# Performance work log

Hardware: AMD Instinct MI355X
Metric: run time of the kernel (lower is better)

## Reference

```python
import jax, jax.numpy as jnp
import numpy as np

B, T, D, HID, H = 256, 256, 72, 512, 1024


def setup_inputs() -> dict:
    key = jax.random.key(0)
    ks = jax.random.split(key, 21)
    s = 0.02
    w = lambda k, sh: jax.random.normal(k, sh, dtype=jnp.float32) * s
    return {
        "x": jax.random.normal(ks[0], (B, T, D), dtype=jnp.float32),
        "to_predict": 10,
        "p2l_w1": w(ks[1], (HID, D)), "p2l_b1": jnp.zeros((HID,), jnp.float32),
        "p2l_w2": w(ks[2], (H, HID)), "p2l_b2": jnp.zeros((H,), jnp.float32),
        "enc_wih": w(ks[3], (3 * H, H)), "enc_whh": w(ks[4], (3 * H, H)),
        "enc_bih": jnp.zeros((3 * H,), jnp.float32), "enc_bhh": jnp.zeros((3 * H,), jnp.float32),
        "dec_wih": w(ks[5], (3 * H, H)), "dec_whh": w(ks[6], (3 * H, H)),
        "dec_bih": jnp.zeros((3 * H,), jnp.float32), "dec_bhh": jnp.zeros((3 * H,), jnp.float32),
        "l2p_w1": w(ks[7], (HID, H)), "l2p_b1": jnp.zeros((HID,), jnp.float32),
        "l2p_w2": w(ks[8], (D, HID)), "l2p_b2": jnp.zeros((D,), jnp.float32),
        "l2s_w1": w(ks[9], (HID, H)), "l2s_b1": jnp.zeros((HID,), jnp.float32),
        "l2s_w2": w(ks[10], (1, HID)), "l2s_b2": jnp.zeros((1,), jnp.float32),
    }


def _lin(x, w, b):
    return x @ w.T + b


def _gru_gates(gi, gh, h):
    # PyTorch gate order: reset, update, new
    i_r, i_z, i_n = jnp.split(gi, 3, axis=-1)
    h_r, h_z, h_n = jnp.split(gh, 3, axis=-1)
    r = jax.nn.sigmoid(i_r + h_r)
    z = jax.nn.sigmoid(i_z + h_z)
    n = jnp.tanh(i_n + r * h_n)
    return (1.0 - z) * n + z * h


def _forward(x, to_predict,
             p2l_w1, p2l_b1, p2l_w2, p2l_b2,
             enc_wih, enc_whh, enc_bih, enc_bhh,
             dec_wih, dec_whh, dec_bih, dec_bhh,
             l2p_w1, l2p_b1, l2p_w2, l2p_b2,
             l2s_w1, l2s_b1, l2s_w2, l2s_b2):
    par2lat = lambda p: jax.nn.relu(_lin(jax.nn.relu(_lin(p, p2l_w1, p2l_b1)), p2l_w2, p2l_b2))
    lat2par = lambda h: _lin(jax.nn.relu(_lin(h, l2p_w1, l2p_b1)), l2p_w2, l2p_b2)

    latent = par2lat(x)  # [B,T,H]
    # encoder GRU (batch_first, single layer, h0 = 0)
    xp = _lin(latent, enc_wih, enc_bih)  # [B,T,3H] precomputed input projections

    def enc_step(h, gi_t):
        h2 = _gru_gates(gi_t, _lin(h, enc_whh, enc_bhh), h)
        return h2, h2

    h0 = jnp.zeros((x.shape[0], H), latent.dtype)
    _, out = jax.lax.scan(enc_step, h0, jnp.swapaxes(xp, 0, 1))
    output = jnp.swapaxes(out, 0, 1)  # [B,T,H]

    # softmax attention pooling over time
    logits = _lin(jax.nn.relu(_lin(output, l2s_w1, l2s_b1)), l2s_w2, l2s_b2)  # [B,T,1]
    weights = jax.nn.softmax(logits, axis=1)
    Rep = jnp.sum(weights * output, axis=1)  # [B,H]

    def dec_step(carry, _):
        hs, p = carry
        inp = par2lat(p)
        hs = _gru_gates(_lin(inp, dec_wih, dec_bih), _lin(hs, dec_whh, dec_bhh), hs)
        pred = lat2par(hs)
        return (hs, pred), pred

    _, preds = jax.lax.scan(dec_step, (Rep, x[:, -1, :]), None, length=to_predict)
    return jnp.transpose(preds, (1, 0, 2)), Rep  # [B,to_predict,72], [B,H]


def reference(x, to_predict,
              p2l_w1, p2l_b1, p2l_w2, p2l_b2,
              enc_wih, enc_whh, enc_bih, enc_bhh,
              dec_wih, dec_whh, dec_bih, dec_bhh,
              l2p_w1, l2p_b1, l2p_w2, l2p_b2,
              l2s_w1, l2s_b1, l2s_w2, l2s_b2):
    return _forward(x, to_predict,
                    p2l_w1, p2l_b1, p2l_w2, p2l_b2,
                    enc_wih, enc_whh, enc_bih, enc_bhh,
                    dec_wih, dec_whh, dec_bih, dec_bhh,
                    l2p_w1, l2p_b1, l2p_w2, l2p_b2,
                    l2s_w1, l2s_b1, l2s_w2, l2s_b2)
```

## Files before the change

### kernel.cpp

```cpp
#include <hip/hip_runtime.h>
#include <hip/hip_bf16.h>
#include <cstdint>
#include <cstddef>


using bf16 = __hip_bfloat16;
typedef __attribute__((ext_vector_type(8))) short short8;
typedef __attribute__((ext_vector_type(4))) short s4_t;
typedef __attribute__((ext_vector_type(4))) float floatx4;

#define B_    256
#define T_    256
#define D_    72
#define DP_   96
#define HID_  512
#define H_    1024
#define H3_   3072
#define NPRED 10
#define CHUNK 32
#define RA    16384

__device__ __forceinline__ float b2f(bf16 v){ return __bfloat162float(v); }
__device__ __forceinline__ bf16  f2b(float v){ return __float2bfloat16(v); }

__device__ __forceinline__ void async_ld16(const bf16* g, bf16* l) {
  __builtin_amdgcn_global_load_lds(
      (const __attribute__((address_space(1))) unsigned int*)g,
      (__attribute__((address_space(3))) unsigned int*)l,
      16, 0, 0);
}

__device__ __forceinline__ short8 load16_cached(const bf16* p) {
  short8 r;
  asm volatile("global_load_dwordx4 %0, %1, off"
               : "=v"(r) : "v"(p) : "memory");
  return r;
}
__device__ __forceinline__ void store8_llc(bf16* p, s4_t v) {
  asm volatile("global_store_dwordx2 %0, %1, off sc0 sc1"
               :: "v"(p), "v"(v) : "memory");
}

enum { EPI_F32 = 0, EPI_BF16 = 1, EPI_BF16_RELU = 2, EPI_BF16_RELU_PERM = 3 };

template<int BM, int BN, int WM, int WN, int EPI>
__global__ __launch_bounds__(256, 2) void gemm_bt(
    const bf16* __restrict__ A, const bf16* __restrict__ B,
    const float* __restrict__ bias, void* __restrict__ Cout,
    int M, int N, int K, int row_off)
{
  constexpr int BK = 32;
  constexpr int NWN = BN / WN;
  constexpr int MT = WM / 16, NT = WN / 16;
  constexpr int ASEG = BM * 4;
  constexpr int TSEG = (BM + BN) * 4;
  static_assert((BM/WM)*(BN/WN) == 4, "4 waves");
  static_assert(TSEG % 256 == 0, "uniform staging");

  __shared__ __align__(16) bf16 smem[(BM + BN) * BK];
  bf16* As = smem;
  bf16* Bs = smem + BM * BK;

  const int tid  = threadIdx.x;
  const int lane = tid & 63;
  const int wave = tid >> 6;
  const int wm = wave / NWN, wn = wave % NWN;
  const int m0 = blockIdx.y * BM, n0 = blockIdx.x * BN;

  floatx4 acc[MT][NT];
#pragma unroll
  for (int i = 0; i < MT; i++)
#pragma unroll
    for (int j = 0; j < NT; j++)
      acc[i][j] = floatx4{0.f, 0.f, 0.f, 0.f};

  const int krow = (lane >> 4) << 3;
  const int r16  = lane & 15;

  for (int k0 = 0; k0 < K; k0 += BK) {
    __syncthreads();
#pragma unroll
    for (int it = 0; it < TSEG / 256; it++) {
      int s = tid + it * 256;
      const bf16* g;
      if (s < ASEG) {
        int row = s >> 2, kseg = s & 3;
        g = A + (size_t)(m0 + row) * K + k0 + kseg * 8;
      } else {
        int s2 = s - ASEG;
        int row = s2 >> 2, kseg = s2 & 3;
        g = B + (size_t)(n0 + row) * K + k0 + kseg * 8;
      }
      async_ld16(g, smem + (size_t)s * 8);
    }
    __syncthreads();
    short8 af[MT], bfr[NT];
#pragma unroll
    for (int i = 0; i < MT; i++)
      af[i] = *(const short8*)(As + (wm * WM + i * 16 + r16) * BK + krow);
#pragma unroll
    for (int j = 0; j < NT; j++)
      bfr[j] = *(const short8*)(Bs + (wn * WN + j * 16 + r16) * BK + krow);
#pragma unroll
    for (int i = 0; i < MT; i++)
#pragma unroll
      for (int j = 0; j < NT; j++)
        acc[i][j] = __builtin_amdgcn_mfma_f32_16x16x32_bf16(af[i], bfr[j], acc[i][j], 0, 0, 0);
  }

#pragma unroll
  for (int i = 0; i < MT; i++) {
#pragma unroll
    for (int j = 0; j < NT; j++) {
      int gn = n0 + wn * WN + j * 16 + r16;
      float bv = bias ? bias[gn] : 0.f;
#pragma unroll
      for (int r = 0; r < 4; r++) {
        int gm = m0 + wm * WM + i * 16 + ((lane >> 4) << 2) + r;
        float v = acc[i][j][r] + bv;
        if (EPI == EPI_BF16_RELU || EPI == EPI_BF16_RELU_PERM) v = fmaxf(v, 0.f);
        size_t orow;
        if (EPI == EPI_BF16_RELU_PERM) {
          int g = row_off + gm;
          orow = (size_t)(g & 255) * 256 + (size_t)(g >> 8);
        } else {
          orow = (size_t)gm;
        }
        if (EPI == EPI_F32) ((float*)Cout)[orow * (size_t)N + gn] = v;
        else                ((bf16*) Cout)[orow * (size_t)N + gn] = f2b(v);
      }
    }
  }
}

__global__ __launch_bounds__(256, 2) void gemm_bt_dual(
    const bf16* __restrict__ A0, const bf16* __restrict__ B0,
    const float* __restrict__ bias0, float* __restrict__ C0,
    const bf16* __restrict__ A1, const bf16* __restrict__ B1,
    const float* __restrict__ bias1, float* __restrict__ C1,
    int M, int N, int K)
{
  constexpr int BM = 64, BN = 128, BK = 32;
  constexpr int ASEG = BM * 4, TSEG = (BM + BN) * 4;
  const bf16* A = blockIdx.z ? A1 : A0;
  const bf16* B = blockIdx.z ? B1 : B0;
  const float* bias = blockIdx.z ? bias1 : bias0;
  float* Cout = blockIdx.z ? C1 : C0;

  __shared__ __align__(16) bf16 smem[(BM + BN) * BK];
  bf16* As = smem;
  bf16* Bs = smem + BM * BK;

  const int tid  = threadIdx.x;
  const int lane = tid & 63;
  const int wave = tid >> 6;
  const int wm = wave >> 1, wn = wave & 1;
  const int m0 = blockIdx.y * BM, n0 = blockIdx.x * BN;

  floatx4 acc[2][4];
#pragma unroll
  for (int i = 0; i < 2; i++)
#pragma unroll
    for (int j = 0; j < 4; j++)
      acc[i][j] = floatx4{0.f, 0.f, 0.f, 0.f};

  const int krow = (lane >> 4) << 3;
  const int r16  = lane & 15;

  for (int k0 = 0; k0 < K; k0 += BK) {
    __syncthreads();
#pragma unroll
    for (int it = 0; it < TSEG / 256; it++) {
      int s = tid + it * 256;
      const bf16* g;
      if (s < ASEG) {
        int row = s >> 2, kseg = s & 3;
        g = A + (size_t)(m0 + row) * K + k0 + kseg * 8;
      } else {
        int s2 = s - ASEG;
        int row = s2 >> 2, kseg = s2 & 3;
        g = B + (size_t)(n0 + row) * K + k0 + kseg * 8;
      }
      async_ld16(g, smem + (size_t)s * 8);
    }
    __syncthreads();
    short8 af[2], bfr[4];
#pragma unroll
    for (int i = 0; i < 2; i++)
      af[i] = *(const short8*)(As + (wm * 32 + i * 16 + r16) * BK + krow);
#pragma unroll
    for (int j = 0; j < 4; j++)
      bfr[j] = *(const short8*)(Bs + (wn * 64 + j * 16 + r16) * BK + krow);
#pragma unroll
    for (int i = 0; i < 2; i++)
#pragma unroll
      for (int j = 0; j < 4; j++)
        acc[i][j] = __builtin_amdgcn_mfma_f32_16x16x32_bf16(af[i], bfr[j], acc[i][j], 0, 0, 0);
  }

#pragma unroll
  for (int i = 0; i < 2; i++)
#pragma unroll
    for (int j = 0; j < 4; j++) {
      int gn = n0 + wn * 64 + j * 16 + r16;
      float bv = bias[gn];
#pragma unroll
      for (int r = 0; r < 4; r++) {
        int gm = m0 + wm * 32 + i * 16 + ((lane >> 4) << 2) + r;
        Cout[(size_t)gm * N + gn] = acc[i][j][r] + bv;
      }
    }
}

__global__ __launch_bounds__(256, 2) void score_gemm(
    const bf16* __restrict__ A,
    const bf16* __restrict__ Bw,
    const float* __restrict__ b1,
    const float* __restrict__ w2,
    float* __restrict__ part)
{
  constexpr int BK = 32;
  __shared__ __align__(16) bf16 smem[(128 + 128) * BK];
  __shared__ float pl[128][33];
  bf16* As = smem;
  bf16* Bs = smem + 128 * BK;

  const int tid  = threadIdx.x;
  const int lane = tid & 63;
  const int wave = tid >> 6;
  const int wm = wave >> 1, wn = wave & 1;
  const int m0 = blockIdx.y * 128, n0 = blockIdx.x * 128;
  const int krow = (lane >> 4) << 3;
  const int r16  = lane & 15;
  const int kq   = lane >> 4;

  floatx4 acc[4][4];
#pragma unroll
  for (int i = 0; i < 4; i++)
#pragma unroll
    for (int j = 0; j < 4; j++)
      acc[i][j] = floatx4{0.f, 0.f, 0.f, 0.f};

  for (int k0 = 0; k0 < H_; k0 += BK) {
    __syncthreads();
#pragma unroll
    for (int it = 0; it < 4; it++) {
      int s = tid + it * 256;
      const bf16* g;
      if (s < 512) {
        int row = s >> 2, kseg = s & 3;
        g = A + (size_t)(m0 + row) * H_ + k0 + kseg * 8;
      } else {
        int s2 = s - 512;
        int row = s2 >> 2, kseg = s2 & 3;
        g = Bw + (size_t)(n0 + row) * H_ + k0 + kseg * 8;
      }
      async_ld16(g, smem + (size_t)s * 8);
    }
    __syncthreads();
    short8 af[4], bfr[4];
#pragma unroll
    for (int i = 0; i < 4; i++)
      af[i] = *(const short8*)(As + (wm * 64 + i * 16 + r16) * BK + krow);
#pragma unroll
    for (int j = 0; j < 4; j++)
      bfr[j] = *(const short8*)(Bs + (wn * 64 + j * 16 + r16) * BK + krow);
#pragma unroll
    for (int i = 0; i < 4; i++)
#pragma unroll
      for (int j = 0; j < 4; j++)
        acc[i][j] = __builtin_amdgcn_mfma_f32_16x16x32_bf16(af[i], bfr[j], acc[i][j], 0, 0, 0);
  }

#pragma unroll
  for (int i = 0; i < 4; i++) {
#pragma unroll
    for (int r = 0; r < 4; r++) {
      int row = wm * 64 + i * 16 + kq * 4 + r;
      float s = 0.f;
#pragma unroll
      for (int j = 0; j < 4; j++) {
        int gn = n0 + wn * 64 + j * 16 + r16;
        s += fmaxf(acc[i][j][r] + b1[gn], 0.f) * w2[gn];
      }
      pl[row][wn * 16 + r16] = s;
    }
  }
  __syncthreads();
  if (tid < 128) {
    float t = 0.f;
#pragma unroll
    for (int c = 0; c < 32; c++) t += pl[tid][c];
    part[(size_t)(m0 + tid) * 4 + blockIdx.x] = t;
  }
}

__global__ void logits_red(const float* __restrict__ part, float* __restrict__ logit)
{
  int i = blockIdx.x * blockDim.x + threadIdx.x;
  logit[i] = part[(size_t)i * 4] + part[(size_t)i * 4 + 1]
           + part[(size_t)i * 4 + 2] + part[(size_t)i * 4 + 3];
}

__global__ void convert_pad(const float* __restrict__ in, bf16* __restrict__ out,
                            int rows, int kin, int kout)
{
  size_t idx = (size_t)blockIdx.x * blockDim.x + threadIdx.x;
  if (idx >= (size_t)rows * kout) return;
  int r = idx / kout, c = idx % kout;
  out[idx] = (c < kin) ? f2b(in[(size_t)r * kin + c]) : f2b(0.f);
}

__global__ void enc_init(float* __restrict__ h32, unsigned* __restrict__ bar)
{
  int idx = blockIdx.x * blockDim.x + threadIdx.x;
  h32[idx] = 0.f;
  if (idx < 512) bar[idx] = 0u;
}

__global__ void ppad_init(const float* __restrict__ x, bf16* __restrict__ ppad)
{
  int idx = blockIdx.x * blockDim.x + threadIdx.x;
  int b = idx / DP_, c = idx % DP_;
  float v = (c < D_) ? x[((size_t)b * T_ + (T_ - 1)) * D_ + c] : 0.f;
  ppad[idx] = f2b(v);
}

__device__ __forceinline__ float sigm(float v){ return 1.f / (1.f + __expf(-v)); }

#define ENC_SMEM (98304 + 4*64*52*4)
static_assert(ENC_SMEM <= 160*1024, "LDS");

__global__ __launch_bounds__(256, 1) void enc_fused(
    const bf16* __restrict__ xpc_cur,
    const bf16* __restrict__ whh,
    const float* __restrict__ bhh,
    bf16* __restrict__ enc_out,
    float* __restrict__ h32g,
    unsigned* __restrict__ bar,
    int t0,
    const bf16* __restrict__ lat_nxt,
    const bf16* __restrict__ wih,
    const float* __restrict__ bih,
    bf16* __restrict__ xpc_nxt)
{
  extern __shared__ char smem[];
  const int tid  = threadIdx.x;
  const int lane = tid & 63;
  const int wave = tid >> 6;
  const int wg   = blockIdx.x;
  const int r16  = lane & 15;
  const int kq   = lane >> 4;

  if (wg < 128) {
    float* P = (float*)(smem + 98304);
    constexpr int PS = 52;

    const int rgrp = wg >> 5;
    const int rowb = rgrp * 64;
    const int j0   = (wg & 31) * 32;
    const int kb0  = wave * 256;

    unsigned* flagp  = bar + rgrp * 32 + wave * 8 + (lane & 7);
    unsigned* myflag = bar + rgrp * 32 + (wg & 31);

    for (int ci = tid; ci < 48 * 128; ci += 256) {
      int wrow = ci >> 7, kslot = ci & 127;
      int g = wrow >> 4, jj = wrow & 15;
      short8 v = *(const short8*)(whh + ((size_t)(g * H_ + j0 + jj)) * H_ + kslot * 8);
      *(short8*)(smem + kslot * 768 + wrow * 16) = v;
    }
    short8 rw[8][3];
#pragma unroll
    for (int it = 0; it < 8; it++)
#pragma unroll
      for (int g = 0; g < 3; g++)
        rw[it][g] = *(const short8*)(whh + ((size_t)(g * H_ + j0 + 16 + r16)) * H_
                                     + kb0 + it * 32 + kq * 8);

    const int row_loc = tid >> 2;
    const int cq      = tid & 3;
    const int b       = rowb + row_loc;
    const int jb0     = j0 + cq * 4;
    const int jb1     = j0 + 16 + cq * 4;

    floatx4 h32r0 = *(const floatx4*)(h32g + (size_t)b * H_ + jb0);
    floatx4 h32r1 = *(const floatx4*)(h32g + (size_t)b * H_ + jb1);
    const floatx4 bhr0 = *(const floatx4*)(bhh + jb0);
    const floatx4 bhz0 = *(const floatx4*)(bhh + H_ + jb0);
    const floatx4 bhn0 = *(const floatx4*)(bhh + 2 * H_ + jb0);
    const floatx4 bhr1 = *(const floatx4*)(bhh + jb1);
    const floatx4 bhz1 = *(const floatx4*)(bhh + H_ + jb1);
    const floatx4 bhn1 = *(const floatx4*)(bhh + 2 * H_ + jb1);

    __syncthreads();

#define ISSUE(IT)                                                              \
    {                                                                          \
      _Pragma("unroll")                                                        \
      for (int rf = 0; rf < 4; rf++)                                           \
        a[(IT) & 3][rf] = load16_cached(hsrc + (size_t)(rowb + rf * 16 + r16) * H_ \
                                        + kb0 + (IT) * 32 + kq * 8);           \
    }
#define GRP(IT, WC)                                                            \
    do {                                                                       \
      const char* bb = smem + (wave * 32 + (IT) * 4 + kq) * 768 + r16 * 16;    \
      short8 bw0 = *(const short8*)(bb);                                       \
      short8 bw1 = *(const short8*)(bb + 256);                                 \
      short8 bw2 = *(const short8*)(bb + 512);                                 \
      asm volatile("s_waitcnt vmcnt(" #WC ")" ::: "memory");                   \
      __builtin_amdgcn_sched_barrier(0);                                       \
      _Pragma("unroll")                                                        \
      for (int rf = 0; rf < 4; rf++) {                                         \
        accA[rf][0] = __builtin_amdgcn_mfma_f32_16x16x32_bf16(a[(IT)&3][rf], bw0, accA[rf][0], 0, 0, 0); \
        accA[rf][1] = __builtin_amdgcn_mfma_f32_16x16x32_bf16(a[(IT)&3][rf], bw1, accA[rf][1], 0, 0, 0); \
        accA[rf][2] = __builtin_amdgcn_mfma_f32_16x16x32_bf16(a[(IT)&3][rf], bw2, accA[rf][2], 0, 0, 0); \
        accB[rf][0] = __builtin_amdgcn_mfma_f32_16x16x32_bf16(a[(IT)&3][rf], rw[IT][0], accB[rf][0], 0, 0, 0); \
        accB[rf][1] = __builtin_amdgcn_mfma_f32_16x16x32_bf16(a[(IT)&3][rf], rw[IT][1], accB[rf][1], 0, 0, 0); \
        accB[rf][2] = __builtin_amdgcn_mfma_f32_16x16x32_bf16(a[(IT)&3][rf], rw[IT][2], accB[rf][2], 0, 0, 0); \
      }                                                                        \
      if ((IT) + 4 < 8) ISSUE((IT) + 4)                                        \
    } while (0)

    for (int ts = 0; ts < CHUNK; ts++) {
      const int tg = t0 + ts;

      const bf16* gi = xpc_cur + ((size_t)ts * B_ + b) * H3_;
      s4_t vr0 = *(const s4_t*)(gi + jb0);
      s4_t vz0 = *(const s4_t*)(gi + H_ + jb0);
      s4_t vn0 = *(const s4_t*)(gi + 2 * H_ + jb0);
      s4_t vr1 = *(const s4_t*)(gi + jb1);
      s4_t vz1 = *(const s4_t*)(gi + H_ + jb1);
      s4_t vn1 = *(const s4_t*)(gi + 2 * H_ + jb1);

      floatx4 accA[4][3], accB[4][3];
#pragma unroll
      for (int rf = 0; rf < 4; rf++)
#pragma unroll
        for (int g = 0; g < 3; g++) {
          accA[rf][g] = floatx4{0.f, 0.f, 0.f, 0.f};
          accB[rf][g] = floatx4{0.f, 0.f, 0.f, 0.f};
        }

      if (tg > 0) {
        const unsigned tgt = (unsigned)tg;
        while (1) {
          unsigned f;
          asm volatile("global_load_dword %0, %1, off sc0 sc1"
                       : "=v"(f) : "v"(flagp) : "memory");
          asm volatile("s_waitcnt vmcnt(0)" ::: "memory");
          if (__all((int)(f >= tgt))) break;
          __builtin_amdgcn_s_sleep(2);
        }
        const bf16* hsrc = enc_out + (size_t)(tg - 1) * B_ * H_;
        short8 a[4][4];
        ISSUE(0) ISSUE(1) ISSUE(2) ISSUE(3)
        GRP(0, 12); GRP(1, 12); GRP(2, 12); GRP(3, 12);
        GRP(4, 12); GRP(5,  8); GRP(6,  4); GRP(7,  0);
      }

#pragma unroll
      for (int rf = 0; rf < 4; rf++)
#pragma unroll
        for (int g = 0; g < 3; g++)
#pragma unroll
          for (int rr = 0; rr < 4; rr++)
            P[(wave * 64 + rf * 16 + kq * 4 + rr) * PS + g * 16 + r16] = accA[rf][g][rr];
      __syncthreads();
      {
        const float* Pr = P + row_loc * PS + cq * 4;
        floatx4 sr4 = floatx4{0.f,0.f,0.f,0.f};
        floatx4 sz4 = floatx4{0.f,0.f,0.f,0.f};
        floatx4 sn4 = floatx4{0.f,0.f,0.f,0.f};
#pragma unroll
        for (int w = 0; w < 4; w++) {
          const float* pp = Pr + w * 64 * PS;
          sr4 += *(const floatx4*)(pp);
          sz4 += *(const floatx4*)(pp + 16);
          sn4 += *(const floatx4*)(pp + 32);
        }
        s4_t outv;
#pragma unroll
        for (int cc = 0; cc < 4; cc++) {
          float xr = __uint_as_float(((unsigned)(unsigned short)vr0[cc]) << 16);
          float xz = __uint_as_float(((unsigned)(unsigned short)vz0[cc]) << 16);
          float xn = __uint_as_float(((unsigned)(unsigned short)vn0[cc]) << 16);
          float rg = sigm(xr + sr4[cc] + bhr0[cc]);
          float zg = sigm(xz + sz4[cc] + bhz0[cc]);
          float ng = tanhf(xn + rg * (sn4[cc] + bhn0[cc]));
          float hnew = (1.f - zg) * ng + zg * h32r0[cc];
          h32r0[cc] = hnew;
          outv[cc] = (short)__builtin_bit_cast(unsigned short, f2b(hnew));
        }
        store8_llc(enc_out + ((size_t)tg * B_ + b) * H_ + jb0, outv);
      }
      __syncthreads();

#pragma unroll
      for (int rf = 0; rf < 4; rf++)
#pragma unroll
        for (int g = 0; g < 3; g++)
#pragma unroll
          for (int rr = 0; rr < 4; rr++)
            P[(wave * 64 + rf * 16 + kq * 4 + rr) * PS + g * 16 + r16] = accB[rf][g][rr];
      __syncthreads();
      {
        const float* Pr = P + row_loc * PS + cq * 4;
        floatx4 sr4 = floatx4{0.f,0.f,0.f,0.f};
        floatx4 sz4 = floatx4{0.f,0.f,0.f,0.f};
        floatx4 sn4 = floatx4{0.f,0.f,0.f,0.f};
#pragma unroll
        for (int w = 0; w < 4; w++) {
          const float* pp = Pr + w * 64 * PS;
          sr4 += *(const floatx4*)(pp);
          sz4 += *(const floatx4*)(pp + 16);
          sn4 += *(const floatx4*)(pp + 32);
        }
        s4_t outv;
#pragma unroll
        for (int cc = 0; cc < 4; cc++) {
          float xr = __uint_as_float(((unsigned)(unsigned short)vr1[cc]) << 16);
          float xz = __uint_as_float(((unsigned)(unsigned short)vz1[cc]) << 16);
          float xn = __uint_as_float(((unsigned)(unsigned short)vn1[cc]) << 16);
          float rg = sigm(xr + sr4[cc] + bhr1[cc]);
          float zg = sigm(xz + sz4[cc] + bhz1[cc]);
          float ng = tanhf(xn + rg * (sn4[cc] + bhn1[cc]));
          float hnew = (1.f - zg) * ng + zg * h32r1[cc];
          h32r1[cc] = hnew;
          outv[cc] = (short)__builtin_bit_cast(unsigned short, f2b(hnew));
        }
        store8_llc(enc_out + ((size_t)tg * B_ + b) * H_ + jb1, outv);
      }

      asm volatile("s_waitcnt vmcnt(0)" ::: "memory");
      __syncthreads();
      if (tid == 0) {
        unsigned v = (unsigned)(tg + 1);
        asm volatile("global_store_dword %0, %1, off sc0 sc1"
                     :: "v"(myflag), "v"(v) : "memory");
      }
    }
#undef GRP
#undef ISSUE

    *(floatx4*)(h32g + (size_t)b * H_ + jb0) = h32r0;
    *(floatx4*)(h32g + (size_t)b * H_ + jb1) = h32r1;

  } else {
    if (xpc_nxt == nullptr) return;
    const int p  = wg - 128;
    const int wm = wave >> 1, wn = wave & 1;
    bf16* As = (bf16*)smem;
    bf16* Bs = As + 128 * 32;
    const int krow = kq << 3;

    for (int tile = 0; tile < 12; tile++) {
      const int t  = p + tile * 128;
      const int m0 = (t / 24) * 128;
      const int n0 = (t % 24) * 128;

      floatx4 acc[4][4];
#pragma unroll
      for (int i = 0; i < 4; i++)
#pragma unroll
        for (int j = 0; j < 4; j++)
          acc[i][j] = floatx4{0.f, 0.f, 0.f, 0.f};

      for (int k0 = 0; k0 < H_; k0 += 32) {
        __syncthreads();
#pragma unroll
        for (int it = 0; it < 4; it++) {
          int s = tid + it * 256;
          const bf16* g;
          if (s < 512) {
            int row = s >> 2, kseg = s & 3;
            g = lat_nxt + (size_t)(m0 + row) * H_ + k0 + kseg * 8;
          } else {
            int s2 = s - 512;
            int row = s2 >> 2, kseg = s2 & 3;
            g = wih + (size_t)(n0 + row) * H_ + k0 + kseg * 8;
          }
          async_ld16(g, (bf16*)smem + (size_t)s * 8);
        }
        __syncthreads();
        short8 af[4], bfr[4];
#pragma unroll
        for (int i = 0; i < 4; i++)
          af[i] = *(const short8*)(As + (wm * 64 + i * 16 + r16) * 32 + krow);
#pragma unroll
        for (int j = 0; j < 4; j++)
          bfr[j] = *(const short8*)(Bs + (wn * 64 + j * 16 + r16) * 32 + krow);
#pragma unroll
        for (int i = 0; i < 4; i++)
#pragma unroll
          for (int j = 0; j < 4; j++)
            acc[i][j] = __builtin_amdgcn_mfma_f32_16x16x32_bf16(af[i], bfr[j], acc[i][j], 0, 0, 0);
      }

#pragma unroll
      for (int i = 0; i < 4; i++)
#pragma unroll
        for (int j = 0; j < 4; j++) {
          int gn = n0 + wn * 64 + j * 16 + r16;
          float bv = bih[gn];
#pragma unroll
          for (int r = 0; r < 4; r++) {
            int gm = m0 + wm * 64 + i * 16 + (kq << 2) + r;
            xpc_nxt[(size_t)gm * H3_ + gn] = f2b(acc[i][j][r] + bv);
          }
        }
      __syncthreads();
    }
  }
}

__global__ void dec_gates(const float* __restrict__ gi, const float* __restrict__ gh,
                          float* __restrict__ hs32, bf16* __restrict__ hs16)
{
  int idx = blockIdx.x * blockDim.x + threadIdx.x;
  int b = idx >> 10, j = idx & (H_ - 1);
  const float* gir = gi + (size_t)b * H3_;
  const float* ghr = gh + (size_t)b * H3_;
  float r = sigm(gir[j] + ghr[j]);
  float z = sigm(gir[j + H_] + ghr[j + H_]);
  float n = tanhf(gir[j + 2 * H_] + r * ghr[j + 2 * H_]);
  float hnew = (1.f - z) * n + z * hs32[idx];
  hs32[idx] = hnew;
  hs16[idx] = f2b(hnew);
}

__global__ void attention(const float* __restrict__ logits, const bf16* __restrict__ enc_out,
                          float* __restrict__ rep, float* __restrict__ hs32,
                          bf16* __restrict__ hs16)
{
  int b = blockIdx.x, t = threadIdx.x;
  __shared__ float w[T_];
  __shared__ float red[T_];
  float lg = logits[(size_t)t * B_ + b];
  red[t] = lg; __syncthreads();
  for (int s = 128; s > 0; s >>= 1) { if (t < s) red[t] = fmaxf(red[t], red[t + s]); __syncthreads(); }
  float mx = red[0]; __syncthreads();
  float e = __expf(lg - mx);
  w[t] = e; red[t] = e; __syncthreads();
  for (int s = 128; s > 0; s >>= 1) { if (t < s) red[t] += red[t + s]; __syncthreads(); }
  float inv = 1.f / red[0];
  float acc[4] = {0.f, 0.f, 0.f, 0.f};
  for (int tt = 0; tt < T_; tt++) {
    float wt = w[tt] * inv;
    const bf16* row = enc_out + ((size_t)tt * B_ + b) * H_;
#pragma unroll
    for (int i = 0; i < 4; i++) acc[i] += wt * b2f(row[t + i * 256]);
  }
#pragma unroll
  for (int i = 0; i < 4; i++) {
    int j = t + i * 256;
    rep [(size_t)b * H_ + j] = acc[i];
    hs32[(size_t)b * H_ + j] = acc[i];
    hs16[(size_t)b * H_ + j] = f2b(acc[i]);
  }
}

__global__ void pred_k(const bf16* __restrict__ e1, const float* __restrict__ w2,
                       const float* __restrict__ b2, float* __restrict__ out,
                       bf16* __restrict__ ppad, int s)
{
  int b = blockIdx.x, t = threadIdx.x;
  __shared__ float ev[HID_];
  for (int k = t; k < HID_; k += 256) ev[k] = b2f(e1[(size_t)b * HID_ + k]);
  __syncthreads();
  if (t < D_) {
    float acc = b2[t];
    const float* wr = w2 + (size_t)t * HID_;
    for (int k = 0; k < HID_; k++) acc += ev[k] * wr[k];
    out[(size_t)b * (NPRED * D_) + s * D_ + t] = acc;
    ppad[b * DP_ + t] = f2b(acc);
  }
}

extern "C" void kernel_launch(void* const* d_in, const int* in_sizes, int n_in,
                              void* d_out, int out_size, void* d_ws, size_t ws_size,
                              hipStream_t stream)
{
  const float* x       = (const float*)d_in[0];
  const float* p2l_w1  = (const float*)d_in[2];
  const float* p2l_b1  = (const float*)d_in[3];
  const float* p2l_w2  = (const float*)d_in[4];
  const float* p2l_b2  = (const float*)d_in[5];
  const float* enc_wih = (const float*)d_in[6];
  const float* enc_whh = (const float*)d_in[7];
  const float* enc_bih = (const float*)d_in[8];
  const float* enc_bhh = (const float*)d_in[9];
  const float* dec_wih = (const float*)d_in[10];
  const float* dec_whh = (const float*)d_in[11];
  const float* dec_bih = (const float*)d_in[12];
  const float* dec_bhh = (const float*)d_in[13];
  const float* l2p_w1  = (const float*)d_in[14];
  const float* l2p_b1  = (const float*)d_in[15];
  const float* l2p_w2  = (const float*)d_in[16];
  const float* l2p_b2  = (const float*)d_in[17];
  const float* l2s_w1  = (const float*)d_in[18];
  const float* l2s_b1  = (const float*)d_in[19];
  const float* l2s_w2  = (const float*)d_in[20];
  const float* l2s_b2  = (const float*)d_in[21];
  (void)l2s_b2;

  float* out_preds = (float*)d_out;
  float* out_rep   = (float*)d_out + (size_t)B_ * NPRED * D_;

  char* p = (char*)d_ws;
  auto alloc = [&](size_t bytes) -> char* {
    char* r = p; p += (bytes + 255) & ~(size_t)255; return r;
  };
  bf16* w_p2l1 = (bf16*)alloc((size_t)HID_ * DP_ * 2);
  bf16* w_p2l2 = (bf16*)alloc((size_t)H_ * HID_ * 2);
  bf16* w_ewih = (bf16*)alloc((size_t)H3_ * H_ * 2);
  bf16* w_ewhh = (bf16*)alloc((size_t)H3_ * H_ * 2);
  bf16* w_l2p1 = (bf16*)alloc((size_t)HID_ * H_ * 2);
  bf16* w_l2s1 = (bf16*)alloc((size_t)HID_ * H_ * 2);
  bf16* latent = (bf16*)alloc((size_t)B_ * T_ * H_ * 2);
  bf16* xpcA   = (bf16*)alloc((size_t)CHUNK * B_ * H3_ * 2);
  bf16* xpcB   = (bf16*)alloc((size_t)CHUNK * B_ * H3_ * 2);
  float* h32  = (float*)alloc((size_t)B_ * H_ * 4);
  float* hs32 = (float*)alloc((size_t)B_ * H_ * 4);
  bf16*  hs16 = (bf16*) alloc((size_t)B_ * H_ * 2);
  float* logit= (float*)alloc((size_t)B_ * T_ * 4);
  bf16*  d1   = (bf16*) alloc((size_t)B_ * HID_ * 2);
  bf16*  inp  = (bf16*) alloc((size_t)B_ * H_ * 2);
  bf16*  e1   = (bf16*) alloc((size_t)B_ * HID_ * 2);
  bf16*  ppad = (bf16*) alloc((size_t)B_ * DP_ * 2);
  unsigned* bar = (unsigned*)alloc(2048);
  bf16*  enc_out = latent;

  bf16* xb    = xpcB;
  bf16* tmpc  = xpcB + (size_t)B_ * T_ * DP_;
  float* part_g = (float*)xpcB;
  float* ghb  = (float*)(xpcA + (size_t)8 * 1024 * 1024);
  float* gib  = ghb + (size_t)B_ * H3_;
  bf16* w_dwih = xpcB;
  bf16* w_dwhh = xpcB + (size_t)H3_ * H_;

  if ((size_t)(p - (char*)d_ws) > ws_size) return;

  const int TB = B_ * T_;

  auto cgrid = [](size_t n) { return dim3((unsigned)((n + 255) / 256)); };
  convert_pad<<<cgrid((size_t)TB * DP_),   256, 0, stream>>>(x,       xb,     TB,   D_,   DP_);
  convert_pad<<<cgrid((size_t)HID_ * DP_), 256, 0, stream>>>(p2l_w1,  w_p2l1, HID_, D_,   DP_);
  convert_pad<<<cgrid((size_t)H_ * HID_),  256, 0, stream>>>(p2l_w2,  w_p2l2, H_,   HID_, HID_);
  convert_pad<<<cgrid((size_t)H3_ * H_),   256, 0, stream>>>(enc_wih, w_ewih, H3_,  H_,   H_);
  convert_pad<<<cgrid((size_t)H3_ * H_),   256, 0, stream>>>(enc_whh, w_ewhh, H3_,  H_,   H_);
  convert_pad<<<cgrid((size_t)HID_ * H_),  256, 0, stream>>>(l2p_w1,  w_l2p1, HID_, H_,   H_);
  convert_pad<<<cgrid((size_t)HID_ * H_),  256, 0, stream>>>(l2s_w1,  w_l2s1, HID_, H_,   H_);

  for (int rc = 0; rc < TB / RA; rc++) {
    { dim3 g(HID_ / 128, RA / 128);
      gemm_bt<128,128,64,64,EPI_BF16_RELU><<<g, 256, 0, stream>>>(
          xb + (size_t)rc * RA * DP_, w_p2l1, p2l_b1, tmpc, RA, HID_, DP_, 0); }
    { dim3 g(H_ / 128, RA / 128);
      gemm_bt<128,128,64,64,EPI_BF16_RELU_PERM><<<g, 256, 0, stream>>>(
          tmpc, w_p2l2, p2l_b2, latent, RA, H_, HID_, rc * RA); }
  }

  (void)hipFuncSetAttribute((const void*)enc_fused,
                            hipFuncAttributeMaxDynamicSharedMemorySize, ENC_SMEM);
  enc_init<<<(B_ * H_) / 256, 256, 0, stream>>>(h32, bar);
  { dim3 g(H3_ / 128, (CHUNK * B_) / 128);
    gemm_bt<128,128,64,64,EPI_BF16><<<g, 256, 0, stream>>>(
        latent, w_ewih, enc_bih, xpcA, CHUNK * B_, H3_, H_, 0); }
  for (int tc = 0; tc < T_ / CHUNK; tc++) {
    bf16* cur = (tc & 1) ? xpcB : xpcA;
    bf16* nxt = (tc < 7) ? ((tc & 1) ? xpcA : xpcB) : nullptr;
    const bf16* latn = latent + (size_t)(tc + 1 < 8 ? tc + 1 : 0) * CHUNK * B_ * H_;
    enc_fused<<<dim3(256), dim3(256), ENC_SMEM, stream>>>(
        cur, w_ewhh, enc_bhh, enc_out, h32, bar, tc * CHUNK,
        latn, w_ewih, enc_bih, nxt);
  }

  score_gemm<<<dim3(4, TB / 128), 256, 0, stream>>>(
      enc_out, w_l2s1, l2s_b1, l2s_w2, part_g);
  logits_red<<<TB / 256, 256, 0, stream>>>(part_g, logit);
  attention<<<B_, 256, 0, stream>>>(logit, enc_out, out_rep, hs32, hs16);

  convert_pad<<<cgrid((size_t)H3_ * H_), 256, 0, stream>>>(dec_wih, w_dwih, H3_, H_, H_);
  convert_pad<<<cgrid((size_t)H3_ * H_), 256, 0, stream>>>(dec_whh, w_dwhh, H3_, H_, H_);
  ppad_init<<<(B_ * DP_) / 256, 256, 0, stream>>>(x, ppad);
  for (int s = 0; s < NPRED; s++) {
    { dim3 g(HID_ / 128, B_ / 64);
      gemm_bt<64,128,32,64,EPI_BF16_RELU><<<g, 256, 0, stream>>>(ppad, w_p2l1, p2l_b1, d1, B_, HID_, DP_, 0); }
    { dim3 g(H_ / 128, B_ / 64);
      gemm_bt<64,128,32,64,EPI_BF16_RELU><<<g, 256, 0, stream>>>(d1, w_p2l2, p2l_b2, inp, B_, H_, HID_, 0); }
    { dim3 g(H3_ / 128, B_ / 64, 2);
      gemm_bt_dual<<<g, 256, 0, stream>>>(inp, w_dwih, dec_bih, gib,
                                          hs16, w_dwhh, dec_bhh, ghb, B_, H3_, H_); }
    dec_gates<<<(B_ * H_) / 256, 256, 0, stream>>>(gib, ghb, hs32, hs16);
    { dim3 g(HID_ / 128, B_ / 64);
      gemm_bt<64,128,32,64,EPI_BF16_RELU><<<g, 256, 0, stream>>>(hs16, w_l2p1, l2p_b1, e1, B_, HID_, H_, 0); }
    pred_k<<<B_, 256, 0, stream>>>(e1, l2p_w2, l2p_b2, out_preds, ppad, s);
  }
}
```

Measured before the change: 3.242 ms.

## Overlap attention score GEMM and decoder weight conversion with encoder recurrence

Producer blocks of the fused encoder kernel now compute the attention-score GEMM tiles for the previous chunk while consumer blocks run the recurrence. During the last chunk they also convert the decoder weights to bf16. This leaves only the final chunk's score tiles for a standalone launch, and the separate logits reduction is folded into the attention kernel. The aim is to hide score and conversion work behind the latency-bound GRU loop. The cost is that producer blocks get more work, which may delay the next chunk's input projections or contend for memory bandwidth with the recurrence.

```diff
diff --git a/kernel.cpp b/kernel.cpp
--- a/kernel.cpp
+++ b/kernel.cpp
@@ -212,24 +212,19 @@
     }
 }
 
-__global__ __launch_bounds__(256, 2) void score_gemm(
-    const bf16* __restrict__ A,
-    const bf16* __restrict__ Bw,
-    const float* __restrict__ b1,
-    const float* __restrict__ w2,
-    float* __restrict__ part)
+__device__ __forceinline__ void score_tile(
+    char* sm, const bf16* __restrict__ A, const bf16* __restrict__ Bw,
+    const float* __restrict__ b1, const float* __restrict__ w2,
+    float* __restrict__ part, size_t m0, int n0, int tid)
 {
   constexpr int BK = 32;
-  __shared__ __align__(16) bf16 smem[(128 + 128) * BK];
-  __shared__ float pl[128][33];
-  bf16* As = smem;
-  bf16* Bs = smem + 128 * BK;
-
-  const int tid  = threadIdx.x;
+  bf16* As = (bf16*)sm;
+  bf16* Bs = As + 128 * BK;
+  float* pl = (float*)(sm + 16384);
+
   const int lane = tid & 63;
   const int wave = tid >> 6;
   const int wm = wave >> 1, wn = wave & 1;
-  const int m0 = blockIdx.y * 128, n0 = blockIdx.x * 128;
   const int krow = (lane >> 4) << 3;
   const int r16  = lane & 15;
   const int kq   = lane >> 4;
@@ -249,13 +244,13 @@
       const bf16* g;
       if (s < 512) {
         int row = s >> 2, kseg = s & 3;
-        g = A + (size_t)(m0 + row) * H_ + k0 + kseg * 8;
+        g = A + (m0 + row) * H_ + k0 + kseg * 8;
       } else {
         int s2 = s - 512;
         int row = s2 >> 2, kseg = s2 & 3;
         g = Bw + (size_t)(n0 + row) * H_ + k0 + kseg * 8;
       }
-      async_ld16(g, smem + (size_t)s * 8);
+      async_ld16(g, As + (size_t)s * 8);
     }
     __syncthreads();
     short8 af[4], bfr[4];
@@ -283,23 +278,28 @@
         int gn = n0 + wn * 64 + j * 16 + r16;
         s += fmaxf(acc[i][j][r] + b1[gn], 0.f) * w2[gn];
       }
-      pl[row][wn * 16 + r16] = s;
+      pl[row * 33 + wn * 16 + r16] = s;
     }
   }
   __syncthreads();
   if (tid < 128) {
     float t = 0.f;
 #pragma unroll
-    for (int c = 0; c < 32; c++) t += pl[tid][c];
-    part[(size_t)(m0 + tid) * 4 + blockIdx.x] = t;
-  }
-}
-
-__global__ void logits_red(const float* __restrict__ part, float* __restrict__ logit)
-{
-  int i = blockIdx.x * blockDim.x + threadIdx.x;
-  logit[i] = part[(size_t)i * 4] + part[(size_t)i * 4 + 1]
-           + part[(size_t)i * 4 + 2] + part[(size_t)i * 4 + 3];
+    for (int c = 0; c < 32; c++) t += pl[tid * 33 + c];
+    part[(m0 + tid) * 4 + (n0 >> 7)] = t;
+  }
+  __syncthreads();
+}
+
+__global__ __launch_bounds__(256, 2) void score_gemm(
+    const bf16* __restrict__ A, const bf16* __restrict__ Bw,
+    const float* __restrict__ b1, const float* __restrict__ w2,
+    float* __restrict__ part, int m_off)
+{
+  __shared__ __align__(16) char sbuf[33536];
+  score_tile(sbuf, A, Bw, b1, w2, part,
+             (size_t)m_off + (size_t)blockIdx.y * 128, blockIdx.x * 128,
+             threadIdx.x);
 }
 
 __global__ void convert_pad(const float* __restrict__ in, bf16* __restrict__ out,
@@ -330,6 +330,7 @@
 
 #define ENC_SMEM (98304 + 4*64*52*4)
 static_assert(ENC_SMEM <= 160*1024, "LDS");
+static_assert(ENC_SMEM >= 33536, "producer score smem fits");
 
 __global__ __launch_bounds__(256, 1) void enc_fused(
     const bf16* __restrict__ xpc_cur,
@@ -342,7 +343,15 @@
     const bf16* __restrict__ lat_nxt,
     const bf16* __restrict__ wih,
     const float* __restrict__ bih,
-    bf16* __restrict__ xpc_nxt)
+    bf16* __restrict__ xpc_nxt,
+    const bf16* __restrict__ sw1,
+    const float* __restrict__ sb1,
+    const float* __restrict__ sw2,
+    float* __restrict__ part,
+    const float* __restrict__ dwih_f,
+    const float* __restrict__ dwhh_f,
+    bf16* __restrict__ dwih_b,
+    bf16* __restrict__ dwhh_b)
 {
   extern __shared__ char smem[];
   const int tid  = threadIdx.x;
@@ -547,69 +556,90 @@
     *(floatx4*)(h32g + (size_t)b * H_ + jb1) = h32r1;
 
   } else {
-    if (xpc_nxt == nullptr) return;
-    const int p  = wg - 128;
-    const int wm = wave >> 1, wn = wave & 1;
-    bf16* As = (bf16*)smem;
-    bf16* Bs = As + 128 * 32;
-    const int krow = kq << 3;
-
-    for (int tile = 0; tile < 12; tile++) {
-      const int t  = p + tile * 128;
-      const int m0 = (t / 24) * 128;
-      const int n0 = (t % 24) * 128;
-
-      floatx4 acc[4][4];
-#pragma unroll
-      for (int i = 0; i < 4; i++)
-#pragma unroll
-        for (int j = 0; j < 4; j++)
-          acc[i][j] = floatx4{0.f, 0.f, 0.f, 0.f};
-
-      for (int k0 = 0; k0 < H_; k0 += 32) {
+    const int p = wg - 128;
+
+    if (xpc_nxt != nullptr) {
+      const int wm = wave >> 1, wn = wave & 1;
+      bf16* As = (bf16*)smem;
+      bf16* Bs = As + 128 * 32;
+      const int krow = kq << 3;
+
+      for (int tile = 0; tile < 12; tile++) {
+        const int t  = p + tile * 128;
+        const int m0 = (t / 24) * 128;
+        const int n0 = (t % 24) * 128;
+
+        floatx4 acc[4][4];
+#pragma unroll
+        for (int i = 0; i < 4; i++)
+#pragma unroll
+          for (int j = 0; j < 4; j++)
+            acc[i][j] = floatx4{0.f, 0.f, 0.f, 0.f};
+
+        for (int k0 = 0; k0 < H_; k0 += 32) {
+          __syncthreads();
+#pragma unroll
+          for (int it = 0; it < 4; it++) {
+            int s = tid + it * 256;
+            const bf16* g;
+            if (s < 512) {
+              int row = s >> 2, kseg = s & 3;
+              g = lat_nxt + (size_t)(m0 + row) * H_ + k0 + kseg * 8;
+            } else {
+              int s2 = s - 512;
+              int row = s2 >> 2, kseg = s2 & 3;
+              g = wih + (size_t)(n0 + row) * H_ + k0 + kseg * 8;
+            }
+            async_ld16(g, (bf16*)smem + (size_t)s * 8);
+          }
+          __syncthreads();
+          short8 af[4], bfr[4];
+#pragma unroll
+          for (int i = 0; i < 4; i++)
+            af[i] = *(const short8*)(As + (wm * 64 + i * 16 + r16) * 32 + krow);
+#pragma unroll
+          for (int j = 0; j < 4; j++)
+            bfr[j] = *(const short8*)(Bs + (wn * 64 + j * 16 + r16) * 32 + krow);
+#pragma unroll
+          for (int i = 0; i < 4; i++)
+#pragma unroll
+            for (int j = 0; j < 4; j++)
+              acc[i][j] = __builtin_amdgcn_mfma_f32_16x16x32_bf16(af[i], bfr[j], acc[i][j], 0, 0, 0);
+        }
+
+#pragma unroll
+        for (int i = 0; i < 4; i++)
+#pragma unroll
+          for (int j = 0; j < 4; j++) {
+            int gn = n0 + wn * 64 + j * 16 + r16;
+            float bv = bih[gn];
+#pragma unroll
+            for (int r = 0; r < 4; r++) {
+              int gm = m0 + wm * 64 + i * 16 + (kq << 2) + r;
+              xpc_nxt[(size_t)gm * H3_ + gn] = f2b(acc[i][j][r] + bv);
+            }
+          }
         __syncthreads();
-#pragma unroll
-        for (int it = 0; it < 4; it++) {
-          int s = tid + it * 256;
-          const bf16* g;
-          if (s < 512) {
-            int row = s >> 2, kseg = s & 3;
-            g = lat_nxt + (size_t)(m0 + row) * H_ + k0 + kseg * 8;
-          } else {
-            int s2 = s - 512;
-            int row = s2 >> 2, kseg = s2 & 3;
-            g = wih + (size_t)(n0 + row) * H_ + k0 + kseg * 8;
-          }
-          async_ld16(g, (bf16*)smem + (size_t)s * 8);
-        }
-        __syncthreads();
-        short8 af[4], bfr[4];
-#pragma unroll
-        for (int i = 0; i < 4; i++)
-          af[i] = *(const short8*)(As + (wm * 64 + i * 16 + r16) * 32 + krow);
-#pragma unroll
-        for (int j = 0; j < 4; j++)
-          bfr[j] = *(const short8*)(Bs + (wn * 64 + j * 16 + r16) * 32 + krow);
-#pragma unroll
-        for (int i = 0; i < 4; i++)
-#pragma unroll
-          for (int j = 0; j < 4; j++)
-            acc[i][j] = __builtin_amdgcn_mfma_f32_16x16x32_bf16(af[i], bfr[j], acc[i][j], 0, 0, 0);
-      }
-
-#pragma unroll
-      for (int i = 0; i < 4; i++)
-#pragma unroll
-        for (int j = 0; j < 4; j++) {
-          int gn = n0 + wn * 64 + j * 16 + r16;
-          float bv = bih[gn];
-#pragma unroll
-          for (int r = 0; r < 4; r++) {
-            int gm = m0 + wm * 64 + i * 16 + (kq << 2) + r;
-            xpc_nxt[(size_t)gm * H3_ + gn] = f2b(acc[i][j][r] + bv);
-          }
-        }
-      __syncthreads();
+      }
+    }
+
+    if (t0 >= CHUNK) {
+      const size_t crow = (size_t)(t0 - CHUNK) * B_;
+#pragma unroll
+      for (int q = 0; q < 2; q++) {
+        int t  = p + q * 128;
+        int rb = t >> 2, cb = t & 3;
+        score_tile(smem, enc_out, sw1, sb1, sw2, part,
+                   crow + (size_t)rb * 128, cb * 128, tid);
+      }
+    }
+
+    if (dwih_f != nullptr) {
+      const size_t N = (size_t)H3_ * H_;
+      for (size_t i = (size_t)p * 256 + tid; i < N; i += 128 * 256) {
+        dwih_b[i] = f2b(dwih_f[i]);
+        dwhh_b[i] = f2b(dwhh_f[i]);
+      }
     }
   }
 }
@@ -629,14 +659,15 @@
   hs16[idx] = f2b(hnew);
 }
 
-__global__ void attention(const float* __restrict__ logits, const bf16* __restrict__ enc_out,
+__global__ void attention(const float* __restrict__ part, const bf16* __restrict__ enc_out,
                           float* __restrict__ rep, float* __restrict__ hs32,
                           bf16* __restrict__ hs16)
 {
   int b = blockIdx.x, t = threadIdx.x;
   __shared__ float w[T_];
   __shared__ float red[T_];
-  float lg = logits[(size_t)t * B_ + b];
+  const float* pr = part + ((size_t)t * B_ + b) * 4;
+  float lg = pr[0] + pr[1] + pr[2] + pr[3];
   red[t] = lg; __syncthreads();
   for (int s = 128; s > 0; s >>= 1) { if (t < s) red[t] = fmaxf(red[t], red[t + s]); __syncthreads(); }
   float mx = red[0]; __syncthreads();
@@ -715,15 +746,17 @@
   bf16* w_p2l2 = (bf16*)alloc((size_t)H_ * HID_ * 2);
   bf16* w_ewih = (bf16*)alloc((size_t)H3_ * H_ * 2);
   bf16* w_ewhh = (bf16*)alloc((size_t)H3_ * H_ * 2);
+  bf16* w_dwih = (bf16*)alloc((size_t)H3_ * H_ * 2);
+  bf16* w_dwhh = (bf16*)alloc((size_t)H3_ * H_ * 2);
   bf16* w_l2p1 = (bf16*)alloc((size_t)HID_ * H_ * 2);
   bf16* w_l2s1 = (bf16*)alloc((size_t)HID_ * H_ * 2);
   bf16* latent = (bf16*)alloc((size_t)B_ * T_ * H_ * 2);
   bf16* xpcA   = (bf16*)alloc((size_t)CHUNK * B_ * H3_ * 2);
   bf16* xpcB   = (bf16*)alloc((size_t)CHUNK * B_ * H3_ * 2);
+  float* part_g= (float*)alloc((size_t)B_ * T_ * 4 * 4);
   float* h32  = (float*)alloc((size_t)B_ * H_ * 4);
   float* hs32 = (float*)alloc((size_t)B_ * H_ * 4);
   bf16*  hs16 = (bf16*) alloc((size_t)B_ * H_ * 2);
-  float* logit= (float*)alloc((size_t)B_ * T_ * 4);
   bf16*  d1   = (bf16*) alloc((size_t)B_ * HID_ * 2);
   bf16*  inp  = (bf16*) alloc((size_t)B_ * H_ * 2);
   bf16*  e1   = (bf16*) alloc((size_t)B_ * HID_ * 2);
@@ -733,11 +766,8 @@
 
   bf16* xb    = xpcB;
   bf16* tmpc  = xpcB + (size_t)B_ * T_ * DP_;
-  float* part_g = (float*)xpcB;
   float* ghb  = (float*)(xpcA + (size_t)8 * 1024 * 1024);
   float* gib  = ghb + (size_t)B_ * H3_;
-  bf16* w_dwih = xpcB;
-  bf16* w_dwhh = xpcB + (size_t)H3_ * H_;
 
   if ((size_t)(p - (char*)d_ws) > ws_size) return;
 
@@ -771,18 +801,18 @@
     bf16* cur = (tc & 1) ? xpcB : xpcA;
     bf16* nxt = (tc < 7) ? ((tc & 1) ? xpcA : xpcB) : nullptr;
     const bf16* latn = latent + (size_t)(tc + 1 < 8 ? tc + 1 : 0) * CHUNK * B_ * H_;
+    const bool last = (tc == 7);
     enc_fused<<<dim3(256), dim3(256), ENC_SMEM, stream>>>(
         cur, w_ewhh, enc_bhh, enc_out, h32, bar, tc * CHUNK,
-        latn, w_ewih, enc_bih, nxt);
-  }
-
-  score_gemm<<<dim3(4, TB / 128), 256, 0, stream>>>(
-      enc_out, w_l2s1, l2s_b1, l2s_w2, part_g);
-  logits_red<<<TB / 256, 256, 0, stream>>>(part_g, logit);
-  attention<<<B_, 256, 0, stream>>>(logit, enc_out, out_rep, hs32, hs16);
-
-  convert_pad<<<cgrid((size_t)H3_ * H_), 256, 0, stream>>>(dec_wih, w_dwih, H3_, H_, H_);
-  convert_pad<<<cgrid((size_t)H3_ * H_), 256, 0, stream>>>(dec_whh, w_dwhh, H3_, H_, H_);
+        latn, w_ewih, enc_bih, nxt,
+        w_l2s1, l2s_b1, l2s_w2, part_g,
+        last ? dec_wih : nullptr, last ? dec_whh : nullptr, w_dwih, w_dwhh);
+  }
+
+  score_gemm<<<dim3(4, 64), 256, 0, stream>>>(
+      enc_out, w_l2s1, l2s_b1, l2s_w2, part_g, 7 * CHUNK * B_);
+  attention<<<B_, 256, 0, stream>>>(part_g, enc_out, out_rep, hs32, hs16);
+
   ppad_init<<<(B_ * DP_) / 256, 256, 0, stream>>>(x, ppad);
   for (int s = 0; s < NPRED; s++) {
     { dim3 g(HID_ / 128, B_ / 64);
```

Measured after the change: 3.368 ms. 1.04x slower.
